# Optimization experiments

Hardware: AMD Instinct MI355X
Metric: run time of the kernel (lower is better)

The kernel has to match this reference:

```python
import jax, jax.numpy as jnp
import numpy as np

N_NODES = 150000
N_ETYPES = 1000
B = 16384
D_CONT = 2
N_NCAT = 3
NCAT_CARD = 64
NCAT_DIM = 16
ETYPE_DIM = 32
N_ECAT = 2
ECAT_CARD = 32
ECAT_DIM = 16
T_DIM = 16
D_IN = D_CONT + N_NCAT * NCAT_DIM      # 50
H = 128                                 # gnn_hidden_dim
P_IN = 2 * H + ETYPE_DIM + N_ECAT * ECAT_DIM + T_DIM  # 336
P_HID = 64


def setup_inputs() -> dict:
    key = jax.random.key(0)
    ks = jax.random.split(key, 24)
    s = 0.05
    inp = {
        "src_node_ids": jax.random.randint(ks[0], (B,), 0, N_NODES),
        "dst_node_ids": jax.random.randint(ks[1], (B,), 0, N_NODES),
        "edge_type_ids": jax.random.randint(ks[2], (B,), 0, N_ETYPES),
        "t_rel": jax.random.uniform(ks[3], (B, 1), dtype=jnp.float32),
        "node_cont": jax.random.normal(ks[4], (N_NODES, D_CONT), dtype=jnp.float32),
        "node_cat_codes": jax.random.randint(ks[5], (N_NCAT, N_NODES), 0, NCAT_CARD),
        "edge_cat_codes": jax.random.randint(ks[6], (N_ECAT, N_ETYPES), 0, ECAT_CARD),
        "edge_index": jax.random.randint(ks[7], (2, 1500000), 0, N_NODES),
        "h_prev": jax.random.normal(ks[8], (N_NODES, H), dtype=jnp.float32),
        "c_prev": jax.random.normal(ks[9], (N_NODES, H), dtype=jnp.float32),
        # learned parameters
        "node_cat_emb": jax.random.normal(ks[10], (N_NCAT, NCAT_CARD, NCAT_DIM), dtype=jnp.float32) * s,
        "edge_id_emb": jax.random.normal(ks[11], (N_ETYPES, ETYPE_DIM), dtype=jnp.float32) * s,
        "edge_cat_emb": jax.random.normal(ks[12], (N_ECAT, ECAT_CARD, ECAT_DIM), dtype=jnp.float32) * s,
        "time_W": jax.random.normal(ks[13], (1, T_DIM), dtype=jnp.float32) * s,
        "time_b": jnp.zeros((T_DIM,), dtype=jnp.float32),
        # GConvLSTM (ChebConv K=1 per gate): gates ordered [i, f, c, o]
        "Wx": jax.random.normal(ks[14], (4, D_IN, H), dtype=jnp.float32) * s,
        "Wh": jax.random.normal(ks[15], (4, H, H), dtype=jnp.float32) * s,
        "b_gate": jnp.zeros((4, H), dtype=jnp.float32),
        "w_c": jax.random.normal(ks[16], (3, H), dtype=jnp.float32) * s,  # peephole for i, f, o
        "W1": jax.random.normal(ks[17], (P_IN, P_HID), dtype=jnp.float32) * s,
        "b1": jnp.zeros((P_HID,), dtype=jnp.float32),
        "W2": jax.random.normal(ks[18], (P_HID, 1), dtype=jnp.float32) * s,
        "b2": jnp.zeros((1,), dtype=jnp.float32),
    }
    return inp


def reference(src_node_ids, dst_node_ids, edge_type_ids, t_rel, node_cont,
              node_cat_codes, edge_cat_codes, edge_index, h_prev, c_prev,
              node_cat_emb, edge_id_emb, edge_cat_emb, time_W, time_b,
              Wx, Wh, b_gate, w_c, W1, b1, W2, b2):
    # --- process node features: cont + 3 categorical embedding gathers ---
    # node_cat_emb[f, node_cat_codes[f, n]] -> [N_NCAT, N, NCAT_DIM]
    cat_e = node_cat_emb[jnp.arange(N_NCAT)[:, None], node_cat_codes]
    cat_e = jnp.transpose(cat_e, (1, 0, 2)).reshape(N_NODES, N_NCAT * NCAT_DIM)
    x = jnp.concatenate([node_cont, cat_e], axis=-1)  # [N, D_IN]

    # --- process batch edge-type features ---
    eid_e = edge_id_emb[edge_type_ids]                               # [B, 32]
    codes_b = edge_cat_codes[:, edge_type_ids]                       # [N_ECAT, B]
    ecat_e = edge_cat_emb[jnp.arange(N_ECAT)[:, None], codes_b]      # [N_ECAT, B, 16]
    ecat_e = jnp.transpose(ecat_e, (1, 0, 2)).reshape(-1, N_ECAT * ECAT_DIM)
    edge_feat = jnp.concatenate([eid_e, ecat_e], axis=-1)            # [B, 64]

    # --- time encoding ---
    t = t_rel if t_rel.ndim == 2 else t_rel[:, None]
    time_e = t @ time_W + time_b                                     # [B, 16]

    # --- GConvLSTM step. ChebConv with K=1: out = x @ W0 + b (T_0(L)x = x),
    # so edge_index is mathematically unused. Gates: [i, f, c_tilde, o]. ---
    z = (jnp.einsum('nd,gdh->gnh', x, Wx)
         + jnp.einsum('nh,ghk->gnk', h_prev, Wh)
         + b_gate[:, None, :])                                       # [4, N, H]
    i_g = jax.nn.sigmoid(z[0] + w_c[0] * c_prev)
    f_g = jax.nn.sigmoid(z[1] + w_c[1] * c_prev)
    t_g = jnp.tanh(z[2])
    c_new = f_g * c_prev + i_g * t_g
    o_g = jax.nn.sigmoid(z[3] + w_c[2] * c_new)
    h_new = o_g * jnp.tanh(c_new)

    # --- link predictor ---
    src_e = h_new[src_node_ids]                                      # [B, H]
    dst_e = h_new[dst_node_ids]                                      # [B, H]
    comb = jnp.concatenate([src_e, dst_e, edge_feat, time_e], axis=-1)  # [B, 336]
    hid = jax.nn.relu(comb @ W1 + b1)
    prob = jax.nn.sigmoid(hid @ W2 + b2)[:, 0]                       # [B]
    return prob, h_new, c_new
```

## Files before the change

kernel.cpp:

```cpp
#include <hip/hip_runtime.h>

#define N_NODES   150000
#define N_PAD     150016
#define B_EDGES   16384
#define H         128
#define KP        192
#define N_NCAT    3
#define NCAT_CARD 64
#define NCAT_DIM  16
#define N_ETYPES  1000
#define ETYPE_DIM 32
#define N_ECAT    2
#define ECAT_CARD 32
#define ECAT_DIM  16
#define T_DIM     16
#define P_IN      336
#define P_HID     64

typedef __bf16 bf16x8 __attribute__((ext_vector_type(8)));
typedef float  f32x4  __attribute__((ext_vector_type(4)));
typedef unsigned int u32x4 __attribute__((ext_vector_type(4)));

__device__ __forceinline__ float rcp_(float x)      { return __builtin_amdgcn_rcpf(x); }
__device__ __forceinline__ float sigmoidf_(float x) { return rcp_(1.0f + __expf(-x)); }
__device__ __forceinline__ float tanhf_(float x)    { return 1.0f - 2.0f * rcp_(__expf(2.0f * x) + 1.0f); }
__device__ __forceinline__ unsigned short f2bf(float f) {
    unsigned u = __float_as_uint(f);
    u += 0x7fffu + ((u >> 16) & 1u);
    return (unsigned short)(u >> 16);
}

__global__ __launch_bounds__(192) void build_w_kernel(
    const float* __restrict__ Wx, const float* __restrict__ Wh,
    unsigned short* __restrict__ Wt)
{
    const int c = blockIdx.x, k = threadIdx.x;
    const int m16 = c & 15;
    const int g   = (c >> 4) & 3;
    const int w   = (c >> 6) & 3;
    const int cbh = c >> 8;
    const int h   = cbh * 64 + w * 16 + m16;
    float v = 0.0f;
    if (k < 50)       v = Wx[(g * 50 + k) * H + h];
    else if (k < 178) v = Wh[(g * H + (k - 50)) * H + h];
    Wt[c * KP + k] = f2bf(v);
}

__global__ __launch_bounds__(512, 4) void lstm_mfma_fused(
    const float* __restrict__ node_cont,
    const int*   __restrict__ node_cat_codes,
    const float* __restrict__ node_cat_emb,
    const float* __restrict__ h_prev,
    const unsigned short* __restrict__ Wt,
    const float* __restrict__ c_prev,
    const float* __restrict__ b_gate,
    const float* __restrict__ w_c,
    float* __restrict__ h_out,
    float* __restrict__ c_out)
{
    __shared__ __align__(16) unsigned short Asub[6 * 64 * 32];

    const int t     = threadIdx.x;
    const int nbase = blockIdx.x * 64;

    {
        const int brow  = t >> 3;
        const int bsub  = t & 7;
        const int bnode = nbase + brow;
        const bool valid = bnode < N_NODES;
        #pragma unroll
        for (int s = 0; s < 3; ++s) {
            const int at = bsub + s * 8;
            const int j0 = at * 8;
            float v[8];
            #pragma unroll
            for (int e = 0; e < 8; ++e) {
                const int j = j0 + e;
                float x = 0.0f;
                if (valid) {
                    if (j < 2) {
                        x = node_cont[bnode * 2 + j];
                    } else if (j < 50) {
                        int c = (j - 2) >> 4, d = (j - 2) & 15;
                        int code = node_cat_codes[c * N_NODES + bnode];
                        x = node_cat_emb[(c * NCAT_CARD + code) * NCAT_DIM + d];
                    } else if (j < 178) {
                        x = h_prev[(size_t)bnode * H + (j - 50)];
                    }
                }
                v[e] = x;
            }
            unsigned u[4];
            #pragma unroll
            for (int p = 0; p < 4; ++p)
                u[p] = (unsigned)f2bf(v[2 * p]) | ((unsigned)f2bf(v[2 * p + 1]) << 16);
            const int kc = at >> 2, a = at & 3;
            const int as = a ^ ((brow >> 1) & 3);
            *(u32x4*)&Asub[(kc * 64 + brow) * 32 + as * 8] = *(const u32x4*)u;
        }
    }
    __syncthreads();

    const int wv   = t >> 6, ln = t & 63;
    const int quad = ln >> 4, m16 = ln & 15;
    const int h    = (wv >> 2) * 64 + (wv & 3) * 16 + m16;

    const unsigned short* wptr[4];
    #pragma unroll
    for (int ni = 0; ni < 4; ++ni)
        wptr[ni] = Wt + (size_t)(wv * 64 + ni * 16 + m16) * KP + quad * 8;

    f32x4 acc[4][4];
    #pragma unroll
    for (int i = 0; i < 4; ++i)
        #pragma unroll
        for (int j = 0; j < 4; ++j) acc[i][j] = (f32x4){0.f, 0.f, 0.f, 0.f};

    #pragma unroll
    for (int kc = 0; kc < 6; ++kc) {
        bf16x8 af[4], bf[4];
        #pragma unroll
        for (int mi = 0; mi < 4; ++mi) {
            const int row = mi * 16 + m16;
            const int as  = quad ^ ((row >> 1) & 3);
            af[mi] = *(const bf16x8*)&Asub[(kc * 64 + row) * 32 + as * 8];
        }
        #pragma unroll
        for (int ni = 0; ni < 4; ++ni)
            bf[ni] = *(const bf16x8*)(wptr[ni] + kc * 32);
        #pragma unroll
        for (int mi = 0; mi < 4; ++mi)
            #pragma unroll
            for (int ni = 0; ni < 4; ++ni)
                acc[mi][ni] = __builtin_amdgcn_mfma_f32_16x16x32_bf16(
                    af[mi], bf[ni], acc[mi][ni], 0, 0, 0);
    }

    const float bg0 = b_gate[0 * H + h], bg1 = b_gate[1 * H + h];
    const float bg2 = b_gate[2 * H + h], bg3 = b_gate[3 * H + h];
    const float wc0 = w_c[0 * H + h], wc1 = w_c[1 * H + h], wc2 = w_c[2 * H + h];

    #pragma unroll
    for (int mi = 0; mi < 4; ++mi)
        #pragma unroll
        for (int r = 0; r < 4; ++r) {
            const int node = nbase + mi * 16 + quad * 4 + r;
            if (node < N_NODES) {
                const size_t off = (size_t)node * H + h;
                const float cp = c_prev[off];
                float ig = sigmoidf_(acc[mi][0][r] + bg0 + wc0 * cp);
                float fg = sigmoidf_(acc[mi][1][r] + bg1 + wc1 * cp);
                float tg = tanhf_(acc[mi][2][r] + bg2);
                float cn = fg * cp + ig * tg;
                float og = sigmoidf_(acc[mi][3][r] + bg3 + wc2 * cn);
                h_out[off] = og * tanhf_(cn);
                c_out[off] = cn;
            }
        }
}

__global__ __launch_bounds__(256) void edge_kernel(
    const int*   __restrict__ src,
    const int*   __restrict__ dst,
    const int*   __restrict__ et,
    const float* __restrict__ t_rel,
    const int*   __restrict__ edge_cat_codes,
    const float* __restrict__ edge_id_emb,
    const float* __restrict__ edge_cat_emb,
    const float* __restrict__ time_W,
    const float* __restrict__ time_b,
    const float* __restrict__ W1,
    const float* __restrict__ b1,
    const float* __restrict__ W2,
    const float* __restrict__ b2,
    const float* __restrict__ h_new,
    float* __restrict__ prob)
{
    __shared__ __align__(16) float comb[4][P_IN];
    const int t = threadIdx.x;
    const int el = t >> 6;
    const int j  = t & 63;
    const int e  = blockIdx.x * 4 + el;

    if (e < B_EDGES) {
        const int s = src[e], d = dst[e], ety = et[e];
        comb[el][j]       = h_new[(size_t)s * H + j];
        comb[el][64 + j]  = h_new[(size_t)s * H + 64 + j];
        comb[el][128 + j] = h_new[(size_t)d * H + j];
        comb[el][192 + j] = h_new[(size_t)d * H + 64 + j];
        if (j < 32) {
            comb[el][256 + j] = edge_id_emb[ety * ETYPE_DIM + j];
            int c = j >> 4, dd = j & 15;
            int code = edge_cat_codes[c * N_ETYPES + ety];
            comb[el][288 + j] = edge_cat_emb[(c * ECAT_CARD + code) * ECAT_DIM + dd];
        }
        if (j < T_DIM) comb[el][320 + j] = t_rel[e] * time_W[j] + time_b[j];
    }
    __syncthreads();
    if (e >= B_EDGES) return;

    float h0 = b1[j], h1 = 0.f, h2 = 0.f, h3 = 0.f;
    #pragma unroll 4
    for (int k = 0; k < P_IN; k += 4) {
        float4 cv = *(const float4*)&comb[el][k];
        h0 = fmaf(cv.x, W1[(k + 0) * P_HID + j], h0);
        h1 = fmaf(cv.y, W1[(k + 1) * P_HID + j], h1);
        h2 = fmaf(cv.z, W1[(k + 2) * P_HID + j], h2);
        h3 = fmaf(cv.w, W1[(k + 3) * P_HID + j], h3);
    }
    float hid = fmaxf((h0 + h1) + (h2 + h3), 0.0f);

    float v = hid * W2[j];
    #pragma unroll
    for (int off = 32; off > 0; off >>= 1) v += __shfl_down(v, off);
    if (j == 0) prob[e] = sigmoidf_(v + b2[0]);
}

extern "C" void kernel_launch(void* const* d_in, const int* in_sizes, int n_in,
                              void* d_out, int out_size, void* d_ws, size_t ws_size,
                              hipStream_t stream) {
    const int*   src            = (const int*)  d_in[0];
    const int*   dst            = (const int*)  d_in[1];
    const int*   et             = (const int*)  d_in[2];
    const float* t_rel          = (const float*)d_in[3];
    const float* node_cont      = (const float*)d_in[4];
    const int*   node_cat_codes = (const int*)  d_in[5];
    const int*   edge_cat_codes = (const int*)  d_in[6];
    const float* h_prev         = (const float*)d_in[8];
    const float* c_prev         = (const float*)d_in[9];
    const float* node_cat_emb   = (const float*)d_in[10];
    const float* edge_id_emb    = (const float*)d_in[11];
    const float* edge_cat_emb   = (const float*)d_in[12];
    const float* time_W         = (const float*)d_in[13];
    const float* time_b         = (const float*)d_in[14];
    const float* Wx             = (const float*)d_in[15];
    const float* Wh             = (const float*)d_in[16];
    const float* b_gate         = (const float*)d_in[17];
    const float* w_c            = (const float*)d_in[18];
    const float* W1             = (const float*)d_in[19];
    const float* b1             = (const float*)d_in[20];
    const float* W2             = (const float*)d_in[21];
    const float* b2             = (const float*)d_in[22];

    float* out   = (float*)d_out;
    float* prob  = out;
    float* h_out = out + B_EDGES;
    float* c_out = out + B_EDGES + (size_t)N_NODES * H;

    unsigned short* Wt = (unsigned short*)d_ws;

    build_w_kernel<<<512, 192, 0, stream>>>(Wx, Wh, Wt);

    lstm_mfma_fused<<<N_PAD / 64, 512, 0, stream>>>(
        node_cont, node_cat_codes, node_cat_emb, h_prev, Wt, c_prev,
        b_gate, w_c, h_out, c_out);

    edge_kernel<<<B_EDGES / 4, 256, 0, stream>>>(src, dst, et, t_rel,
                                                 edge_cat_codes, edge_id_emb, edge_cat_emb,
                                                 time_W, time_b, W1, b1, W2, b2,
                                                 h_out, prob);
}
```

Measured before the change: 477.9 us.

## Vectorize h_prev loads, prefetch c_prev, and stage bf16 W1 in shared memory

The LSTM kernel now puts h_prev first in the K layout so each thread reads it with aligned float4 loads. It also prefetches c_prev into registers before the MFMA loop and relaxes the launch-bounds occupancy hint. The edge kernel handles 16 edges per block, converts W1 to bf16 in shared memory, and reuses each weight across four edges per thread, which cuts global W1 traffic. In exchange, every edge block redoes the W1 conversion, the predictor weights lose precision through bf16, and the extra registers for the c_prev prefetch may lower occupancy.

```diff
diff --git a/kernel.cpp b/kernel.cpp
--- a/kernel.cpp
+++ b/kernel.cpp
@@ -20,6 +20,7 @@
 typedef __bf16 bf16x8 __attribute__((ext_vector_type(8)));
 typedef float  f32x4  __attribute__((ext_vector_type(4)));
 typedef unsigned int u32x4 __attribute__((ext_vector_type(4)));
+typedef unsigned int u32x2 __attribute__((ext_vector_type(2)));
 
 __device__ __forceinline__ float rcp_(float x)      { return __builtin_amdgcn_rcpf(x); }
 __device__ __forceinline__ float sigmoidf_(float x) { return rcp_(1.0f + __expf(-x)); }
@@ -28,6 +29,9 @@
     unsigned u = __float_as_uint(f);
     u += 0x7fffu + ((u >> 16) & 1u);
     return (unsigned short)(u >> 16);
+}
+__device__ __forceinline__ float bf2f(unsigned short b) {
+    return __uint_as_float((unsigned)b << 16);
 }
 
 __global__ __launch_bounds__(192) void build_w_kernel(
@@ -41,12 +45,12 @@
     const int cbh = c >> 8;
     const int h   = cbh * 64 + w * 16 + m16;
     float v = 0.0f;
-    if (k < 50)       v = Wx[(g * 50 + k) * H + h];
-    else if (k < 178) v = Wh[(g * H + (k - 50)) * H + h];
+    if (k < 128)      v = Wh[(g * H + k) * H + h];
+    else if (k < 178) v = Wx[(g * 50 + (k - 128)) * H + h];
     Wt[c * KP + k] = f2bf(v);
 }
 
-__global__ __launch_bounds__(512, 4) void lstm_mfma_fused(
+__global__ __launch_bounds__(512, 3) void lstm_mfma_fused(
     const float* __restrict__ node_cont,
     const int*   __restrict__ node_cat_codes,
     const float* __restrict__ node_cat_emb,
@@ -68,24 +72,40 @@
         const int bsub  = t & 7;
         const int bnode = nbase + brow;
         const bool valid = bnode < N_NODES;
-        #pragma unroll
-        for (int s = 0; s < 3; ++s) {
+        const int swz = (brow >> 1) & 3;
+
+        #pragma unroll
+        for (int s = 0; s < 2; ++s) {
             const int at = bsub + s * 8;
-            const int j0 = at * 8;
+            float4 v0 = {0.f,0.f,0.f,0.f}, v1 = {0.f,0.f,0.f,0.f};
+            if (valid) {
+                const float* hp = h_prev + (size_t)bnode * H + at * 8;
+                v0 = *(const float4*)hp;
+                v1 = *(const float4*)(hp + 4);
+            }
+            unsigned u[4];
+            u[0] = (unsigned)f2bf(v0.x) | ((unsigned)f2bf(v0.y) << 16);
+            u[1] = (unsigned)f2bf(v0.z) | ((unsigned)f2bf(v0.w) << 16);
+            u[2] = (unsigned)f2bf(v1.x) | ((unsigned)f2bf(v1.y) << 16);
+            u[3] = (unsigned)f2bf(v1.z) | ((unsigned)f2bf(v1.w) << 16);
+            const int kc = at >> 2, a = at & 3, as = a ^ swz;
+            *(u32x4*)&Asub[(kc * 64 + brow) * 32 + as * 8] = *(const u32x4*)u;
+        }
+
+        {
+            const int at = 16 + bsub;
             float v[8];
             #pragma unroll
             for (int e = 0; e < 8; ++e) {
-                const int j = j0 + e;
+                const int idx = bsub * 8 + e;
                 float x = 0.0f;
                 if (valid) {
-                    if (j < 2) {
-                        x = node_cont[bnode * 2 + j];
-                    } else if (j < 50) {
-                        int c = (j - 2) >> 4, d = (j - 2) & 15;
+                    if (idx < 2) {
+                        x = node_cont[bnode * 2 + idx];
+                    } else if (idx < 50) {
+                        int c = (idx - 2) >> 4, d = (idx - 2) & 15;
                         int code = node_cat_codes[c * N_NODES + bnode];
                         x = node_cat_emb[(c * NCAT_CARD + code) * NCAT_DIM + d];
-                    } else if (j < 178) {
-                        x = h_prev[(size_t)bnode * H + (j - 50)];
                     }
                 }
                 v[e] = x;
@@ -94,21 +114,30 @@
             #pragma unroll
             for (int p = 0; p < 4; ++p)
                 u[p] = (unsigned)f2bf(v[2 * p]) | ((unsigned)f2bf(v[2 * p + 1]) << 16);
-            const int kc = at >> 2, a = at & 3;
-            const int as = a ^ ((brow >> 1) & 3);
+            const int kc = at >> 2, a = at & 3, as = a ^ swz;
             *(u32x4*)&Asub[(kc * 64 + brow) * 32 + as * 8] = *(const u32x4*)u;
         }
     }
-    __syncthreads();
 
     const int wv   = t >> 6, ln = t & 63;
     const int quad = ln >> 4, m16 = ln & 15;
     const int h    = (wv >> 2) * 64 + (wv & 3) * 16 + m16;
 
+    float cpv[4][4];
+    #pragma unroll
+    for (int mi = 0; mi < 4; ++mi)
+        #pragma unroll
+        for (int r = 0; r < 4; ++r) {
+            const int node = nbase + mi * 16 + quad * 4 + r;
+            cpv[mi][r] = (node < N_NODES) ? c_prev[(size_t)node * H + h] : 0.0f;
+        }
+
     const unsigned short* wptr[4];
     #pragma unroll
     for (int ni = 0; ni < 4; ++ni)
         wptr[ni] = Wt + (size_t)(wv * 64 + ni * 16 + m16) * KP + quad * 8;
+
+    __syncthreads();
 
     f32x4 acc[4][4];
     #pragma unroll
@@ -147,7 +176,7 @@
             const int node = nbase + mi * 16 + quad * 4 + r;
             if (node < N_NODES) {
                 const size_t off = (size_t)node * H + h;
-                const float cp = c_prev[off];
+                const float cp = cpv[mi][r];
                 float ig = sigmoidf_(acc[mi][0][r] + bg0 + wc0 * cp);
                 float fg = sigmoidf_(acc[mi][1][r] + bg1 + wc1 * cp);
                 float tg = tanhf_(acc[mi][2][r] + bg2);
@@ -159,6 +188,7 @@
         }
 }
 
+#define CPAD 340
 __global__ __launch_bounds__(256) void edge_kernel(
     const int*   __restrict__ src,
     const int*   __restrict__ dst,
@@ -176,44 +206,88 @@
     const float* __restrict__ h_new,
     float* __restrict__ prob)
 {
-    __shared__ __align__(16) float comb[4][P_IN];
+    __shared__ __align__(16) unsigned short W1s[P_IN * P_HID];
+    __shared__ __align__(16) float comb[16][CPAD];
+
     const int t = threadIdx.x;
-    const int el = t >> 6;
-    const int j  = t & 63;
-    const int e  = blockIdx.x * 4 + el;
-
+
+    #pragma unroll
+    for (int i = 0; i < 21; ++i) {
+        const int idx = (i * 256 + t) * 4;
+        float4 w = *(const float4*)&W1[idx];
+        unsigned u[2];
+        u[0] = (unsigned)f2bf(w.x) | ((unsigned)f2bf(w.y) << 16);
+        u[1] = (unsigned)f2bf(w.z) | ((unsigned)f2bf(w.w) << 16);
+        *(u32x2*)&W1s[idx] = *(const u32x2*)u;
+    }
+
+    const int el = t >> 4, p = t & 15;
+    const int e  = blockIdx.x * 16 + el;
     if (e < B_EDGES) {
         const int s = src[e], d = dst[e], ety = et[e];
-        comb[el][j]       = h_new[(size_t)s * H + j];
-        comb[el][64 + j]  = h_new[(size_t)s * H + 64 + j];
-        comb[el][128 + j] = h_new[(size_t)d * H + j];
-        comb[el][192 + j] = h_new[(size_t)d * H + 64 + j];
-        if (j < 32) {
-            comb[el][256 + j] = edge_id_emb[ety * ETYPE_DIM + j];
-            int c = j >> 4, dd = j & 15;
-            int code = edge_cat_codes[c * N_ETYPES + ety];
-            comb[el][288 + j] = edge_cat_emb[(c * ECAT_CARD + code) * ECAT_DIM + dd];
-        }
-        if (j < T_DIM) comb[el][320 + j] = t_rel[e] * time_W[j] + time_b[j];
+        const float tr = t_rel[e];
+        const float* hp = (p < 8) ? (h_new + (size_t)s * H + p * 16)
+                                  : (h_new + (size_t)d * H + (p - 8) * 16);
+        #pragma unroll
+        for (int q = 0; q < 4; ++q)
+            *(float4*)&comb[el][p * 16 + q * 4] = *(const float4*)(hp + q * 4);
+        #pragma unroll
+        for (int q = 0; q < 5; ++q) {
+            const int f = p + q * 16;
+            float x;
+            if (f < 32) {
+                x = edge_id_emb[ety * ETYPE_DIM + f];
+            } else if (f < 64) {
+                int c = (f - 32) >> 4, dd = (f - 32) & 15;
+                int code = edge_cat_codes[c * N_ETYPES + ety];
+                x = edge_cat_emb[(c * ECAT_CARD + code) * ECAT_DIM + dd];
+            } else {
+                x = tr * time_W[f - 64] + time_b[f - 64];
+            }
+            comb[el][256 + f] = x;
+        }
     }
     __syncthreads();
-    if (e >= B_EDGES) return;
-
-    float h0 = b1[j], h1 = 0.f, h2 = 0.f, h3 = 0.f;
+
+    const int wv = t >> 6, j = t & 63;
+    const int ebase = blockIdx.x * 16 + wv * 4;
+    float a0 = b1[j], a1 = b1[j], a2 = b1[j], a3 = b1[j];
+    const float* c0 = comb[wv * 4 + 0];
+    const float* c1 = comb[wv * 4 + 1];
+    const float* c2 = comb[wv * 4 + 2];
+    const float* c3 = comb[wv * 4 + 3];
     #pragma unroll 4
-    for (int k = 0; k < P_IN; k += 4) {
-        float4 cv = *(const float4*)&comb[el][k];
-        h0 = fmaf(cv.x, W1[(k + 0) * P_HID + j], h0);
-        h1 = fmaf(cv.y, W1[(k + 1) * P_HID + j], h1);
-        h2 = fmaf(cv.z, W1[(k + 2) * P_HID + j], h2);
-        h3 = fmaf(cv.w, W1[(k + 3) * P_HID + j], h3);
-    }
-    float hid = fmaxf((h0 + h1) + (h2 + h3), 0.0f);
-
-    float v = hid * W2[j];
-    #pragma unroll
-    for (int off = 32; off > 0; off >>= 1) v += __shfl_down(v, off);
-    if (j == 0) prob[e] = sigmoidf_(v + b2[0]);
+    for (int k4 = 0; k4 < P_IN; k4 += 4) {
+        float4 v0 = *(const float4*)&c0[k4];
+        float4 v1 = *(const float4*)&c1[k4];
+        float4 v2 = *(const float4*)&c2[k4];
+        float4 v3 = *(const float4*)&c3[k4];
+        #pragma unroll
+        for (int kk = 0; kk < 4; ++kk) {
+            const float w = bf2f(W1s[(k4 + kk) * P_HID + j]);
+            const float* pv0 = (const float*)&v0;
+            const float* pv1 = (const float*)&v1;
+            const float* pv2 = (const float*)&v2;
+            const float* pv3 = (const float*)&v3;
+            a0 = fmaf(pv0[kk], w, a0);
+            a1 = fmaf(pv1[kk], w, a1);
+            a2 = fmaf(pv2[kk], w, a2);
+            a3 = fmaf(pv3[kk], w, a3);
+        }
+    }
+    const float w2 = W2[j];
+    float v;
+    #define REDUCE_WRITE(ACC, EOFF)                                   \
+        v = fmaxf(ACC, 0.0f) * w2;                                    \
+        _Pragma("unroll")                                             \
+        for (int off = 32; off > 0; off >>= 1) v += __shfl_down(v, off); \
+        if (j == 0 && (ebase + EOFF) < B_EDGES)                       \
+            prob[ebase + EOFF] = sigmoidf_(v + b2[0]);
+    REDUCE_WRITE(a0, 0)
+    REDUCE_WRITE(a1, 1)
+    REDUCE_WRITE(a2, 2)
+    REDUCE_WRITE(a3, 3)
+    #undef REDUCE_WRITE
 }
 
 extern "C" void kernel_launch(void* const* d_in, const int* in_sizes, int n_in,
@@ -255,8 +329,8 @@
         node_cont, node_cat_codes, node_cat_emb, h_prev, Wt, c_prev,
         b_gate, w_c, h_out, c_out);
 
-    edge_kernel<<<B_EDGES / 4, 256, 0, stream>>>(src, dst, et, t_rel,
-                                                 edge_cat_codes, edge_id_emb, edge_cat_emb,
-                                                 time_W, time_b, W1, b1, W2, b2,
-                                                 h_out, prob);
-}
+    edge_kernel<<<B_EDGES / 16, 256, 0, stream>>>(src, dst, et, t_rel,
+                                                  edge_cat_codes, edge_id_emb, edge_cat_emb,
+                                                  time_W, time_b, W1, b1, W2, b2,
+                                                  h_out, prob);
+}
```

Result: faster. 440.1 us (-7.9%).
